# Performance work log

Measured on AMD Instinct MI355X. Metric: run time of the kernel, lower is better.

Reference implementation:

```python
import jax, jax.numpy as jnp
import numpy as np

B, N, E_PER = 512, 256, 8192          # graphs, nodes per graph, edges per graph
FIN, H, K, FOUT = 128, 32, 16, 10     # in_channels, hidden, num clusters, out_channels
EPS = 1e-15


def setup_inputs() -> dict:
    key = jax.random.key(0)
    ks = jax.random.split(key, 12)
    x = jax.random.normal(ks[0], (B * N, FIN), jnp.float32)
    # intra-graph random edges, then offset into the global node index space
    src = jax.random.randint(ks[1], (B, E_PER), 0, N)
    dst = jax.random.randint(ks[2], (B, E_PER), 0, N)
    offs = (jnp.arange(B) * N)[:, None]
    edge_index = jnp.stack([(src + offs).reshape(-1), (dst + offs).reshape(-1)]).astype(jnp.int64)
    batch = jnp.repeat(jnp.arange(B), N).astype(jnp.int64)

    def lin(k, fin, fout):
        return (jax.random.normal(k, (fin, fout), jnp.float32) / np.sqrt(fin)).astype(jnp.float32)

    params = {
        'W_lin1': lin(ks[3], FIN, H), 'b_lin1': jnp.zeros((H,), jnp.float32),
        'W_rel1': lin(ks[4], H, H), 'b_rel1': jnp.zeros((H,), jnp.float32),
        'W_root1': lin(ks[5], H, H),
        'W_pool': lin(ks[6], H, K), 'b_pool': jnp.zeros((K,), jnp.float32),
        'W_rel2': lin(ks[7], H, H), 'b_rel2': jnp.zeros((H,), jnp.float32),
        'W_root2': lin(ks[8], H, H),
        'W_lin2': lin(ks[9], H, H), 'b_lin2': jnp.zeros((H,), jnp.float32),
        'W_lin3': lin(ks[10], H, FOUT), 'b_lin3': jnp.zeros((FOUT,), jnp.float32),
    }
    return {'x': x, 'edge_index': edge_index, 'batch': batch, **params}


def _densify(x, edge_index, batch):
    """to_dense_adj + to_dense_batch: [total,F] -> [B,N,F], [B,N,N], [B,N]."""
    n_total = x.shape[0]
    counts = jax.ops.segment_sum(jnp.ones((n_total,), jnp.int32), batch, num_segments=B)
    offsets = jnp.concatenate([jnp.zeros((1,), jnp.int32), jnp.cumsum(counts)[:-1]])
    pos = jnp.arange(n_total) - offsets[batch]            # position of node inside its graph
    eb = batch[edge_index[0]]                             # graph id of each edge
    adj = jnp.zeros((B, N, N), jnp.float32).at[eb, pos[edge_index[0]], pos[edge_index[1]]].add(1.0)
    xd = jnp.zeros((B, N, x.shape[1]), jnp.float32).at[batch, pos].set(x)
    mask = jnp.zeros((B, N), jnp.float32).at[batch, pos].set(1.0)
    return xd, adj, mask


def _dense_graph_conv(x, adj, W_rel, b_rel, W_root):
    # PyG DenseGraphConv(aggr='add'): lin_rel(adj @ x) + lin_root(x)
    return jnp.einsum('bnm,bmh,hk->bnk', adj, x, W_rel) + b_rel + x @ W_root


def _dense_mincut_pool(x, adj, s, mask):
    s = jax.nn.softmax(s, axis=-1)
    x = x * mask[..., None]
    s = s * mask[..., None]
    out = jnp.einsum('bnk,bnh->bkh', s, x)                        # s^T x
    out_adj = jnp.einsum('bnk,bnm,bmj->bkj', s, adj, s)           # s^T A s
    mincut_num = jnp.einsum('bkk->b', out_adj)
    d_flat = adj.sum(-1)                                          # degree
    mincut_den = jnp.einsum('bnk,bn,bnk->b', s, d_flat, s)        # trace(s^T D s)
    mincut_loss = jnp.mean(-(mincut_num / mincut_den))
    ss = jnp.einsum('bnk,bnj->bkj', s, s)
    ss_norm = jnp.linalg.norm(ss, axis=(-1, -2), keepdims=True)
    i_s = jnp.eye(K, dtype=jnp.float32)
    ortho_loss = jnp.mean(jnp.linalg.norm(ss / ss_norm - i_s / jnp.sqrt(jnp.float32(K)), axis=(-1, -2)))
    # zero diagonal, symmetric degree normalization
    diag_mask = 1.0 - i_s
    out_adj = out_adj * diag_mask
    d = jnp.sqrt(out_adj.sum(-1))[:, None, :] + EPS               # [B,1,K]
    out_adj = out_adj / d / jnp.swapaxes(d, 1, 2)
    return out, out_adj, mincut_loss, ortho_loss


def reference(x, edge_index, batch, W_lin1, b_lin1, W_rel1, b_rel1, W_root1,
              W_pool, b_pool, W_rel2, b_rel2, W_root2, W_lin2, b_lin2, W_lin3, b_lin3):
    xd, adj, mask = _densify(x, edge_index, batch)
    h = xd @ W_lin1 + b_lin1                                      # lin1
    h = _dense_graph_conv(h, adj, W_rel1, b_rel1, W_root1)        # conv1
    s2 = h @ W_pool + b_pool                                      # pool2
    h, adj_p, mincut_loss2, ortho_loss2 = _dense_mincut_pool(h, adj, s2, mask)
    h = _dense_graph_conv(h, adj_p, W_rel2, b_rel2, W_root2)      # conv2
    h = h.sum(axis=1)                                             # readout sum over clusters
    h = jax.nn.relu(h @ W_lin2 + b_lin2)
    h = h @ W_lin3 + b_lin3
    return jax.nn.log_softmax(h, axis=-1), mincut_loss2, ortho_loss2
```

## Files before the change

kernel.cpp:

```cpp
#include <hip/hip_runtime.h>

#define NB 512
#define NN 256
#define EPG 8192
#define FINC 128

typedef float f32x4 __attribute__((ext_vector_type(4)));
typedef short s16x8 __attribute__((ext_vector_type(8)));

__device__ __forceinline__ float bf2f(unsigned short u) {
  union { unsigned int i; float f; } x; x.i = ((unsigned int)u) << 16; return x.f;
}
__device__ __forceinline__ unsigned short f2bf(float f) {
  union { float f; unsigned int i; } x; x.f = f;
  unsigned int r = x.i + 0x7fffu + ((x.i >> 16) & 1u);
  return (unsigned short)(r >> 16);
}
__device__ __forceinline__ short ftrunc_bf(float f) {
  union { float f; unsigned int i; } x; x.f = f;
  return (short)(x.i >> 16);
}

struct Params {
  const void* x; const void* ei;
  const void *wl1, *bl1, *wr1, *br1, *wro1, *wp, *bp;
  const void *wr2, *br2, *wro2, *wl2, *bl2, *wl3, *bl3;
  float* out; float* ws;
};

__device__ __forceinline__ bool detect_bf16(const void* p) {
  const unsigned short* pw = (const unsigned short*)p;
  int sane = 0;
  for (int i = 0; i < 64; ++i) {
    unsigned e = (pw[i] >> 7) & 0xFFu;
    sane += (e > 96u && e < 132u) ? 1 : 0;
  }
  return sane >= 56;
}
__device__ __forceinline__ bool detect_i64(const void* p) {
  const int* pi = (const int*)p + EPG;
  int ok = 0;
  for (int i = 0; i < 32; ++i) ok += (pi[i] >= 256 && pi[i] < 512) ? 1 : 0;
  return ok < 24;
}
__device__ __forceinline__ float ldf(const void* p, int i, bool bf) {
  return bf ? bf2f(((const unsigned short*)p)[i]) : ((const float*)p)[i];
}

#define SMEM_TOTAL 163072

__device__ __forceinline__ float block_sum16(float v, float* scr, int t) {
  #pragma unroll
  for (int o = 32; o > 0; o >>= 1) v += __shfl_xor(v, o, 64);
  __syncthreads();
  if ((t & 63) == 0) scr[t >> 6] = v;
  __syncthreads();
  float s = 0.f;
  #pragma unroll
  for (int i = 0; i < 16; ++i) s += scr[i];
  return s;
}

__global__ __launch_bounds__(1024, 4) void mincut_main(Params P) {
  extern __shared__ char smem[];
  const int t = threadIdx.x;
  const int b = blockIdx.x;

  const bool BF  = detect_bf16(P.wr1);
  const bool I64 = detect_i64(P.ei);

  float* h0buf  = (float*)(smem + 66560);
  unsigned short* taT = (unsigned short*)(smem + 66560);
  unsigned short* sTh = (unsigned short*)(smem + 66560 + 8448);
  unsigned short* sTl = (unsigned short*)(smem + 66560 + 16896);
  float* aggbuf = (float*)(smem + 103424);
  unsigned short* w1th = (unsigned short*)(smem + 103424);
  unsigned short* w1tl = (unsigned short*)(smem + 103424 + 8704);
  unsigned short* h0T  = (unsigned short*)(smem + 140288);
  unsigned short* wrelTh  = (unsigned short*)(smem + 140288);
  unsigned short* wrelTl  = (unsigned short*)(smem + 140288 + 2560);
  unsigned short* wrootTh = (unsigned short*)(smem + 140288 + 5120);
  float* brel1f = (float*)(smem + 140288 + 7680);
  unsigned short* h1Th = (unsigned short*)(smem + 140288);
  unsigned short* poolh = (unsigned short*)(smem + 160768);
  float* bpoolf = (float*)(smem + 160768 + 1024);
  float* blin1f = (float*)(smem + 160768 + 1088);
  float* scr    = (float*)(smem + 160768 + 1216);
  float* degb   = (float*)(smem + 160768 + 1280);
  float* pbuf   = (float*)(smem);
  float* oadjb  = (float*)(smem + 2048);
  float* ssb    = (float*)(smem + 3072);
  float* qbuf   = (float*)(smem + 4096);
  float* ddb    = (float*)(smem + 6144);
  float* h2b    = (float*)(smem + 6208);
  float* rb     = (float*)(smem + 8256);
  float* yb     = (float*)(smem + 8384);
  float* lgb    = (float*)(smem + 8512);
  float* rel2f  = (float*)(smem + 16384);
  float* brel2f = (float*)(smem + 20480);
  float* root2f = (float*)(smem + 20608);
  float* lin2f  = (float*)(smem + 24704);
  float* blin2f = (float*)(smem + 28800);
  float* lin3f  = (float*)(smem + 28928);
  float* blin3f = (float*)(smem + 30208);
  float* pbufH  = (float*)(smem + 40960);
  float* pbufL  = (float*)(smem + 43008);
  float* oadjH  = (float*)(smem + 45056);
  float* oadjL  = (float*)(smem + 46080);
  float* ssA    = (float*)(smem + 47104);
  float* ssB    = (float*)(smem + 48128);
  float* ssC    = (float*)(smem + 49152);

  const int n4 = t >> 2, q4 = t & 3;
  const int wv = t >> 6, lane = t & 63;
  const int lm = lane & 15, quad = lane >> 4;
  const int mbase = wv * 16;

  for (int e = t; e < 4096; e += 1024) {
    int k = e >> 5, c = e & 31;
    float w = ldf(P.wl1, e, BF);
    unsigned short hi = f2bf(w);
    w1th[c * 136 + k] = hi;
    w1tl[c * 136 + k] = f2bf(w - bf2f(hi));
  }
  if (t < 32) blin1f[t] = ldf(P.bl1, t, BF);
  if (t < 512) poolh[t] = f2bf(ldf(P.wp, t, BF));
  if (t < 16) bpoolf[t] = ldf(P.bp, t, BF);
  __syncthreads();

  {
    f32x4 acc[2] = {{0.f,0.f,0.f,0.f},{0.f,0.f,0.f,0.f}};
    const size_t node = (size_t)(b * 256 + mbase + lm);
    #pragma unroll
    for (int ks = 0; ks < 4; ++ks) {
      const int k0 = ks * 32 + quad * 8;
      s16x8 a;
      if (BF) {
        a = *(const s16x8*)((const unsigned short*)P.x + node * 128 + k0);
      } else {
        const float* xp = (const float*)P.x + node * 128 + k0;
        f32x4 v0 = *(const f32x4*)xp;
        f32x4 v1 = *(const f32x4*)(xp + 4);
        #pragma unroll
        for (int j = 0; j < 4; ++j) { a[j] = (short)f2bf(v0[j]); a[4 + j] = (short)f2bf(v1[j]); }
      }
      #pragma unroll
      for (int ct = 0; ct < 2; ++ct) {
        const int c = ct * 16 + lm;
        s16x8 bh = *(const s16x8*)(w1th + c * 136 + k0);
        s16x8 bl = *(const s16x8*)(w1tl + c * 136 + k0);
        acc[ct] = __builtin_amdgcn_mfma_f32_16x16x32_bf16(a, bh, acc[ct], 0, 0, 0);
        acc[ct] = __builtin_amdgcn_mfma_f32_16x16x32_bf16(a, bl, acc[ct], 0, 0, 0);
      }
    }
    #pragma unroll
    for (int ct = 0; ct < 2; ++ct) {
      const int c = ct * 16 + lm;
      float bias = blin1f[c];
      #pragma unroll
      for (int r = 0; r < 4; ++r) {
        int row = mbase + quad * 4 + r;
        float val = acc[ct][r] + bias;
        h0buf[row * 36 + c] = val;
        h0T[c * 264 + row] = f2bf(val);
      }
    }
  }
  __syncthreads();

  {
    uint4 z = {0u, 0u, 0u, 0u};
    for (int i = t; i < 4160; i += 1024) ((uint4*)smem)[i] = z;
  }
  __syncthreads();

  if (I64) {
    const long long* es = (const long long*)P.ei + (size_t)b * EPG;
    const long long* ed = (const long long*)P.ei + (size_t)NB * EPG + (size_t)b * EPG;
    #pragma unroll
    for (int i2 = 0; i2 < 8; ++i2) {
      int e = i2 * 1024 + t;
      unsigned idx = (unsigned)((((int)es[e]) & 255) * 260 + (((int)ed[e]) & 255));
      atomicAdd((unsigned int*)(smem + (idx & ~3u)), 1u << ((idx & 3u) * 8u));
    }
  } else {
    const int* es = (const int*)P.ei + (size_t)b * EPG;
    const int* ed = (const int*)P.ei + (size_t)NB * EPG + (size_t)b * EPG;
    #pragma unroll
    for (int i2 = 0; i2 < 8; ++i2) {
      int e = i2 * 1024 + t;
      unsigned idx = (unsigned)((es[e] & 255) * 260 + (ed[e] & 255));
      atomicAdd((unsigned int*)(smem + (idx & ~3u)), 1u << ((idx & 3u) * 8u));
    }
  }
  __syncthreads();

  s16x8 afr[8];
  {
    f32x4 acc[2] = {{0.f,0.f,0.f,0.f},{0.f,0.f,0.f,0.f}};
    float dsum = 0.f;
    #pragma unroll
    for (int ks = 0; ks < 8; ++ks) {
      const int v0 = ks * 32 + quad * 8;
      const char* ap = smem + (mbase + lm) * 260 + v0;
      unsigned d0 = *(const unsigned int*)(ap);
      unsigned d1 = *(const unsigned int*)(ap + 4);
      s16x8 a;
      #pragma unroll
      for (int j = 0; j < 4; ++j) {
        float f0 = (float)((d0 >> (8 * j)) & 255u);
        float f1 = (float)((d1 >> (8 * j)) & 255u);
        dsum += f0 + f1;
        a[j] = ftrunc_bf(f0);
        a[4 + j] = ftrunc_bf(f1);
      }
      afr[ks] = a;
      #pragma unroll
      for (int ct = 0; ct < 2; ++ct) {
        s16x8 bf = *(const s16x8*)(h0T + (ct * 16 + lm) * 264 + v0);
        acc[ct] = __builtin_amdgcn_mfma_f32_16x16x32_bf16(a, bf, acc[ct], 0, 0, 0);
      }
    }
    #pragma unroll
    for (int ct = 0; ct < 2; ++ct) {
      const int c = ct * 16 + lm;
      #pragma unroll
      for (int r = 0; r < 4; ++r) aggbuf[(mbase + quad * 4 + r) * 36 + c] = acc[ct][r];
    }
    dsum += __shfl_xor(dsum, 16, 64);
    dsum += __shfl_xor(dsum, 32, 64);
    if (lane < 16) degb[mbase + lm] = dsum;
  }
  __syncthreads();

  {
    int k = t >> 5, c = t & 31;
    float wr = ldf(P.wr1, t, BF);
    unsigned short hi = f2bf(wr);
    wrelTh[c * 40 + k] = hi;
    wrelTl[c * 40 + k] = f2bf(wr - bf2f(hi));
    wrootTh[c * 40 + k] = f2bf(ldf(P.wro1, t, BF));
  }
  if (t < 32) brel1f[t] = ldf(P.br1, t, BF);
  __syncthreads();

  f32x4 h1acc[2];
  float bias0, bias1;
  {
    s16x8 Ah, Al, Hh;
    const float* ar = aggbuf + (mbase + lm) * 36 + quad * 8;
    const float* hr = h0buf + (mbase + lm) * 36 + quad * 8;
    #pragma unroll
    for (int j = 0; j < 8; ++j) {
      float f = ar[j];
      unsigned short hi = f2bf(f);
      Ah[j] = (short)hi;
      Al[j] = (short)f2bf(f - bf2f(hi));
      Hh[j] = (short)f2bf(hr[j]);
    }
    bias0 = brel1f[lm]; bias1 = brel1f[16 + lm];
    #pragma unroll
    for (int ct = 0; ct < 2; ++ct) {
      const int c = ct * 16 + lm;
      s16x8 brh = *(const s16x8*)(wrelTh + c * 40 + quad * 8);
      s16x8 brl = *(const s16x8*)(wrelTl + c * 40 + quad * 8);
      s16x8 bwh = *(const s16x8*)(wrootTh + c * 40 + quad * 8);
      f32x4 acc = {0.f, 0.f, 0.f, 0.f};
      acc = __builtin_amdgcn_mfma_f32_16x16x32_bf16(Ah, brh, acc, 0, 0, 0);
      acc = __builtin_amdgcn_mfma_f32_16x16x32_bf16(Ah, brl, acc, 0, 0, 0);
      acc = __builtin_amdgcn_mfma_f32_16x16x32_bf16(Al, brh, acc, 0, 0, 0);
      acc = __builtin_amdgcn_mfma_f32_16x16x32_bf16(Hh, bwh, acc, 0, 0, 0);
      h1acc[ct] = acc;
    }
  }
  __syncthreads();
  {
    #pragma unroll
    for (int ct = 0; ct < 2; ++ct) {
      const int c = ct * 16 + lm;
      float bias = ct ? bias1 : bias0;
      #pragma unroll
      for (int r = 0; r < 4; ++r) {
        int row = mbase + quad * 4 + r;
        float val = h1acc[ct][r] + bias;
        aggbuf[row * 36 + c] = val;
        h1Th[c * 264 + row] = f2bf(val);
      }
    }
  }
  __syncthreads();

  float ssq;
  {
    f32x4 sv = *(const f32x4*)(bpoolf + q4 * 4);
    const float* hrow = aggbuf + n4 * 36;
    #pragma unroll 8
    for (int m = 0; m < 32; ++m) {
      float hm = hrow[m];
      uint2 pw = *(const uint2*)(poolh + m * 16 + q4 * 4);
      sv[0] += hm * bf2f((unsigned short)(pw.x & 0xFFFFu));
      sv[1] += hm * bf2f((unsigned short)(pw.x >> 16));
      sv[2] += hm * bf2f((unsigned short)(pw.y & 0xFFFFu));
      sv[3] += hm * bf2f((unsigned short)(pw.y >> 16));
    }
    float mx = fmaxf(fmaxf(sv[0], sv[1]), fmaxf(sv[2], sv[3]));
    mx = fmaxf(mx, __shfl_xor(mx, 1, 64));
    mx = fmaxf(mx, __shfl_xor(mx, 2, 64));
    #pragma unroll
    for (int i = 0; i < 4; ++i) sv[i] = __expf(sv[i] - mx);
    float sm = sv[0] + sv[1] + sv[2] + sv[3];
    sm += __shfl_xor(sm, 1, 64);
    sm += __shfl_xor(sm, 2, 64);
    float inv = 1.f / sm;
    #pragma unroll
    for (int i = 0; i < 4; ++i) sv[i] *= inv;
    float sq = sv[0] * sv[0] + sv[1] * sv[1] + sv[2] * sv[2] + sv[3] * sv[3];
    sq += __shfl_xor(sq, 1, 64);
    sq += __shfl_xor(sq, 2, 64);
    ssq = sq;
    #pragma unroll
    for (int i = 0; i < 4; ++i) {
      int cl = q4 * 4 + i;
      unsigned short hi = f2bf(sv[i]);
      sTh[cl * 264 + n4] = hi;
      sTl[cl * 264 + n4] = f2bf(sv[i] - bf2f(hi));
    }
  }
  __syncthreads();

  {
    f32x4 tacc = {0.f, 0.f, 0.f, 0.f};
    #pragma unroll
    for (int ks = 0; ks < 8; ++ks) {
      const int v0 = ks * 32 + quad * 8;
      s16x8 bh = *(const s16x8*)(sTh + lm * 264 + v0);
      s16x8 bl = *(const s16x8*)(sTl + lm * 264 + v0);
      tacc = __builtin_amdgcn_mfma_f32_16x16x32_bf16(afr[ks], bh, tacc, 0, 0, 0);
      tacc = __builtin_amdgcn_mfma_f32_16x16x32_bf16(afr[ks], bl, tacc, 0, 0, 0);
    }
    #pragma unroll
    for (int r = 0; r < 4; ++r) taT[lm * 264 + mbase + quad * 4 + r] = f2bf(tacc[r]);
  }
  __syncthreads();

  rel2f[t] = ldf(P.wr2, t, BF);
  if (t < 32) brel2f[t] = ldf(P.br2, t, BF);
  root2f[t] = ldf(P.wro2, t, BF);
  lin2f[t] = ldf(P.wl2, t, BF);
  if (t < 32) blin2f[t] = ldf(P.bl2, t, BF);
  if (t < 320) lin3f[t] = ldf(P.wl3, t, BF);
  if (t < 10) blin3f[t] = ldf(P.bl3, t, BF);

  if (wv < 9) {
    const unsigned short *Ap, *Bp; float* dst; int W, ct = 0;
    switch (wv) {
      case 0: Ap = sTh; Bp = h1Th; dst = pbufH; W = 32; ct = 0; break;
      case 1: Ap = sTh; Bp = h1Th; dst = pbufH; W = 32; ct = 1; break;
      case 2: Ap = sTl; Bp = h1Th; dst = pbufL; W = 32; ct = 0; break;
      case 3: Ap = sTl; Bp = h1Th; dst = pbufL; W = 32; ct = 1; break;
      case 4: Ap = sTh; Bp = taT;  dst = oadjH; W = 16; break;
      case 5: Ap = sTl; Bp = taT;  dst = oadjL; W = 16; break;
      case 6: Ap = sTh; Bp = sTh;  dst = ssA;   W = 16; break;
      case 7: Ap = sTh; Bp = sTl;  dst = ssB;   W = 16; break;
      default: Ap = sTl; Bp = sTh; dst = ssC;   W = 16; break;
    }
    const int cidx = ct * 16 + lm;
    const unsigned short* Bb = Bp + cidx * 264;
    f32x4 acc = {0.f, 0.f, 0.f, 0.f};
    #pragma unroll
    for (int ch = 0; ch < 8; ++ch) {
      s16x8 a = *(const s16x8*)(Ap + lm * 264 + ch * 32 + quad * 8);
      s16x8 bb = *(const s16x8*)(Bb + ch * 32 + quad * 8);
      acc = __builtin_amdgcn_mfma_f32_16x16x32_bf16(a, bb, acc, 0, 0, 0);
    }
    #pragma unroll
    for (int r = 0; r < 4; ++r) dst[(quad * 4 + r) * W + cidx] = acc[r];
  }
  __syncthreads();

  if (t < 512) {
    pbuf[t] = pbufH[t] + pbufL[t];
  } else if (t < 768) {
    int i = t - 512; oadjb[i] = oadjH[i] + oadjL[i];
  } else {
    int i = t - 768; ssb[i] = ssA[i] + ssB[i] + ssC[i];
  }
  __syncthreads();

  {
    float den = block_sum16((q4 == 0) ? degb[n4] * ssq : 0.f, scr, t);
    float num = block_sum16((t < 16) ? oadjb[t * 17] : 0.f, scr, t);
    float fro = block_sum16((t < 256) ? ssb[t] * ssb[t] : 0.f, scr, t);
    float ssn = sqrtf(fro);
    float term = 0.f;
    if (t < 256) {
      float diag = ((t & 15) == (t >> 4)) ? 0.25f : 0.f;
      term = ssb[t] / ssn - diag;
    }
    float orth = block_sum16(term * term, scr, t);
    if (t == 0) {
      atomicAdd(P.ws, -(num / den) * (1.f / NB));
      atomicAdd(P.ws + 1, sqrtf(orth) * (1.f / NB));
    }
  }
  __syncthreads();

  if (t < 16) {
    float rs = 0.f;
    #pragma unroll
    for (int j = 0; j < 16; ++j) if (j != t) rs += oadjb[t * 16 + j];
    ddb[t] = sqrtf(rs) + 1e-15f;
  }
  __syncthreads();
  if (t < 256) {
    int k = t >> 4, j = t & 15;
    float apv = (k == j) ? 0.f : oadjb[t] / (ddb[k] * ddb[j]);
    oadjb[t] = apv;
  }
  __syncthreads();

  if (t < 512) {
    int k = t >> 5, c = t & 31;
    float q = 0.f;
    #pragma unroll
    for (int j = 0; j < 16; ++j) q += oadjb[k * 16 + j] * pbuf[j * 32 + c];
    qbuf[k * 32 + c] = q;
  }
  __syncthreads();
  if (t < 512) {
    int k = t >> 5, c = t & 31;
    float a1 = brel2f[c];
    #pragma unroll
    for (int m = 0; m < 32; ++m)
      a1 += qbuf[k * 32 + m] * rel2f[m * 32 + c] + pbuf[k * 32 + m] * root2f[m * 32 + c];
    h2b[k * 32 + c] = a1;
  }
  __syncthreads();
  if (t < 32) {
    float r = 0.f;
    #pragma unroll
    for (int k = 0; k < 16; ++k) r += h2b[k * 32 + t];
    rb[t] = r;
  }
  __syncthreads();
  if (t < 32) {
    float y = blin2f[t];
    #pragma unroll
    for (int m = 0; m < 32; ++m) y += rb[m] * lin2f[m * 32 + t];
    yb[t] = fmaxf(y, 0.f);
  }
  __syncthreads();
  if (t < 10) {
    float lg = blin3f[t];
    #pragma unroll
    for (int m = 0; m < 32; ++m) lg += yb[m] * lin3f[m * 10 + t];
    lgb[t] = lg;
  }
  __syncthreads();
  if (t == 0) {
    float mx = lgb[0];
    #pragma unroll
    for (int i = 1; i < 10; ++i) mx = fmaxf(mx, lgb[i]);
    float sum = 0.f;
    #pragma unroll
    for (int i = 0; i < 10; ++i) sum += __expf(lgb[i] - mx);
    lgb[10] = mx + __logf(sum);
  }
  __syncthreads();
  if (t < 10) {
    float val = lgb[t] - lgb[10];
    if (BF) ((unsigned short*)P.out)[b * 10 + t] = f2bf(val);
    else    P.out[b * 10 + t] = val;
  }
}

__global__ void mincut_fin(Params P) {
  if (threadIdx.x == 0) {
    const bool BF = detect_bf16(P.wr1);
    if (BF) {
      ((unsigned short*)P.out)[5120] = f2bf(P.ws[0]);
      ((unsigned short*)P.out)[5121] = f2bf(P.ws[1]);
    } else {
      P.out[5120] = P.ws[0];
      P.out[5121] = P.ws[1];
    }
  }
}

extern "C" void kernel_launch(void* const* d_in, const int* in_sizes, int n_in,
                              void* d_out, int out_size, void* d_ws, size_t ws_size,
                              hipStream_t stream) {
  (void)in_sizes; (void)n_in; (void)out_size; (void)ws_size;
  Params P;
  P.x    = d_in[0];
  P.ei   = d_in[1];
  P.wl1  = d_in[3];
  P.bl1  = d_in[4];
  P.wr1  = d_in[5];
  P.br1  = d_in[6];
  P.wro1 = d_in[7];
  P.wp   = d_in[8];
  P.bp   = d_in[9];
  P.wr2  = d_in[10];
  P.br2  = d_in[11];
  P.wro2 = d_in[12];
  P.wl2  = d_in[13];
  P.bl2  = d_in[14];
  P.wl3  = d_in[15];
  P.bl3  = d_in[16];
  P.out  = (float*)d_out;
  P.ws   = (float*)d_ws;

  hipMemsetAsync(d_ws, 0, 2 * sizeof(float), stream);
  hipFuncSetAttribute(reinterpret_cast<const void*>(mincut_main),
                      hipFuncAttributeMaxDynamicSharedMemorySize, SMEM_TOTAL);
  hipLaunchKernelGGL(mincut_main, dim3(NB), dim3(1024), SMEM_TOTAL, stream, P);
  hipLaunchKernelGGL(mincut_fin, dim3(1), dim3(64), 0, stream, P);
}
```

Baseline: 196.5 us.

## Prefetch weights and edges early, MFMA pool softmax, fuse reductions and tail

Weights, biases and edge indices are loaded into registers at kernel start with vectorized edge reads. The adjacency zeroing and atomic scatter move ahead of the lin1 GEMM, which removes a couple of barriers. The pool projection becomes a split-bf16 MFMA with softmax done through wave shuffles. The four loss reductions are fused into a single cross-wave pass, and the ortho loss uses a closed-form trace identity. The classifier tail runs on one wave without block barriers. The adjacency row stride changes to 264, which alters the LDS layout.

```diff
diff --git a/kernel.cpp b/kernel.cpp
--- a/kernel.cpp
+++ b/kernel.cpp
@@ -47,19 +47,7 @@
   return bf ? bf2f(((const unsigned short*)p)[i]) : ((const float*)p)[i];
 }
 
-#define SMEM_TOTAL 163072
-
-__device__ __forceinline__ float block_sum16(float v, float* scr, int t) {
-  #pragma unroll
-  for (int o = 32; o > 0; o >>= 1) v += __shfl_xor(v, o, 64);
-  __syncthreads();
-  if ((t & 63) == 0) scr[t >> 6] = v;
-  __syncthreads();
-  float s = 0.f;
-  #pragma unroll
-  for (int i = 0; i < 16; ++i) s += scr[i];
-  return s;
-}
+#define SMEM_TOTAL 162752
 
 __global__ __launch_bounds__(1024, 4) void mincut_main(Params P) {
   extern __shared__ char smem[];
@@ -69,24 +57,26 @@
   const bool BF  = detect_bf16(P.wr1);
   const bool I64 = detect_i64(P.ei);
 
-  float* h0buf  = (float*)(smem + 66560);
-  unsigned short* taT = (unsigned short*)(smem + 66560);
-  unsigned short* sTh = (unsigned short*)(smem + 66560 + 8448);
-  unsigned short* sTl = (unsigned short*)(smem + 66560 + 16896);
-  float* aggbuf = (float*)(smem + 103424);
-  unsigned short* w1th = (unsigned short*)(smem + 103424);
-  unsigned short* w1tl = (unsigned short*)(smem + 103424 + 8704);
-  unsigned short* h0T  = (unsigned short*)(smem + 140288);
-  unsigned short* wrelTh  = (unsigned short*)(smem + 140288);
-  unsigned short* wrelTl  = (unsigned short*)(smem + 140288 + 2560);
-  unsigned short* wrootTh = (unsigned short*)(smem + 140288 + 5120);
-  float* brel1f = (float*)(smem + 140288 + 7680);
-  unsigned short* h1Th = (unsigned short*)(smem + 140288);
-  unsigned short* poolh = (unsigned short*)(smem + 160768);
-  float* bpoolf = (float*)(smem + 160768 + 1024);
-  float* blin1f = (float*)(smem + 160768 + 1088);
-  float* scr    = (float*)(smem + 160768 + 1216);
-  float* degb   = (float*)(smem + 160768 + 1280);
+  float* h0buf  = (float*)(smem + 67584);
+  unsigned short* taT = (unsigned short*)(smem + 67584);
+  unsigned short* sTh = (unsigned short*)(smem + 76032);
+  unsigned short* sTl = (unsigned short*)(smem + 84480);
+  float* aggbuf = (float*)(smem + 104448);
+  unsigned short* w1th = (unsigned short*)(smem + 104448);
+  unsigned short* w1tl = (unsigned short*)(smem + 113152);
+  unsigned short* h0T  = (unsigned short*)(smem + 141312);
+  unsigned short* wrelTh  = (unsigned short*)(smem + 141312);
+  unsigned short* wrelTl  = (unsigned short*)(smem + 143872);
+  unsigned short* wrootTh = (unsigned short*)(smem + 146432);
+  float* brel1f = (float*)(smem + 148992);
+  unsigned short* h1Th = (unsigned short*)(smem + 141312);
+  unsigned short* poolTh = (unsigned short*)(smem + 158208);
+  unsigned short* poolTl = (unsigned short*)(smem + 159232);
+  float* bpoolf = (float*)(smem + 160256);
+  float* blin1f = (float*)(smem + 160320);
+  float* scr    = (float*)(smem + 160448);
+  float* degb   = (float*)(smem + 160704);
+  float* ssqb   = (float*)(smem + 161728);
   float* pbuf   = (float*)(smem);
   float* oadjb  = (float*)(smem + 2048);
   float* ssb    = (float*)(smem + 3072);
@@ -97,12 +87,9 @@
   float* yb     = (float*)(smem + 8384);
   float* lgb    = (float*)(smem + 8512);
   float* rel2f  = (float*)(smem + 16384);
-  float* brel2f = (float*)(smem + 20480);
   float* root2f = (float*)(smem + 20608);
   float* lin2f  = (float*)(smem + 24704);
-  float* blin2f = (float*)(smem + 28800);
   float* lin3f  = (float*)(smem + 28928);
-  float* blin3f = (float*)(smem + 30208);
   float* pbufH  = (float*)(smem + 40960);
   float* pbufL  = (float*)(smem + 43008);
   float* oadjH  = (float*)(smem + 45056);
@@ -111,11 +98,45 @@
   float* ssB    = (float*)(smem + 48128);
   float* ssC    = (float*)(smem + 49152);
 
-  const int n4 = t >> 2, q4 = t & 3;
   const int wv = t >> 6, lane = t & 63;
   const int lm = lane & 15, quad = lane >> 4;
   const int mbase = wv * 16;
 
+  float wrel_v  = ldf(P.wr1, t, BF);
+  float wroot_v = ldf(P.wro1, t, BF);
+  float brel1_v = (t < 32) ? ldf(P.br1, t, BF) : 0.f;
+  float rel2_v  = ldf(P.wr2, t, BF);
+  float root2_v = ldf(P.wro2, t, BF);
+  float lin2_v  = ldf(P.wl2, t, BF);
+  float lin3_v  = (t < 320) ? ldf(P.wl3, t, BF) : 0.f;
+  float brel2_v = (t < 32) ? ldf(P.br2, t, BF) : 0.f;
+  float blin2_v = (t < 32) ? ldf(P.bl2, t, BF) : 0.f;
+  float blin3_v = (t < 10) ? ldf(P.bl3, t, BF) : 0.f;
+  int eu[8], ev[8];
+  if (I64) {
+    const uint4* s4 = (const uint4*)((const long long*)P.ei + (size_t)b * EPG) + t * 4;
+    const uint4* d4 = (const uint4*)((const long long*)P.ei + (size_t)NB * EPG + (size_t)b * EPG) + t * 4;
+    #pragma unroll
+    for (int i = 0; i < 4; ++i) {
+      uint4 a = s4[i], c = d4[i];
+      eu[2 * i] = a.x & 255; eu[2 * i + 1] = a.z & 255;
+      ev[2 * i] = c.x & 255; ev[2 * i + 1] = c.z & 255;
+    }
+  } else {
+    const uint4* s4 = (const uint4*)((const int*)P.ei + (size_t)b * EPG) + t * 2;
+    const uint4* d4 = (const uint4*)((const int*)P.ei + (size_t)NB * EPG + (size_t)b * EPG) + t * 2;
+    #pragma unroll
+    for (int i = 0; i < 2; ++i) {
+      uint4 a = s4[i], c = d4[i];
+      eu[4 * i] = a.x & 255; eu[4 * i + 1] = a.y & 255; eu[4 * i + 2] = a.z & 255; eu[4 * i + 3] = a.w & 255;
+      ev[4 * i] = c.x & 255; ev[4 * i + 1] = c.y & 255; ev[4 * i + 2] = c.z & 255; ev[4 * i + 3] = c.w & 255;
+    }
+  }
+
+  {
+    uint4 z = {0u, 0u, 0u, 0u};
+    for (int i = t; i < 4224; i += 1024) ((uint4*)smem)[i] = z;
+  }
   for (int e = t; e < 4096; e += 1024) {
     int k = e >> 5, c = e & 31;
     float w = ldf(P.wl1, e, BF);
@@ -123,10 +144,22 @@
     w1th[c * 136 + k] = hi;
     w1tl[c * 136 + k] = f2bf(w - bf2f(hi));
   }
+  if (t < 512) {
+    int m = t >> 4, c = t & 15;
+    float w = ldf(P.wp, t, BF);
+    unsigned short hi = f2bf(w);
+    poolTh[c * 32 + m] = hi;
+    poolTl[c * 32 + m] = f2bf(w - bf2f(hi));
+  }
   if (t < 32) blin1f[t] = ldf(P.bl1, t, BF);
-  if (t < 512) poolh[t] = f2bf(ldf(P.wp, t, BF));
   if (t < 16) bpoolf[t] = ldf(P.bp, t, BF);
   __syncthreads();
+
+  #pragma unroll
+  for (int e = 0; e < 8; ++e) {
+    unsigned idx = (unsigned)(eu[e] * 264 + ev[e]);
+    atomicAdd((unsigned int*)(smem + (idx & ~3u)), 1u << ((idx & 3u) * 8u));
+  }
 
   {
     f32x4 acc[2] = {{0.f,0.f,0.f,0.f},{0.f,0.f,0.f,0.f}};
@@ -168,48 +201,20 @@
   }
   __syncthreads();
 
-  {
-    uint4 z = {0u, 0u, 0u, 0u};
-    for (int i = t; i < 4160; i += 1024) ((uint4*)smem)[i] = z;
-  }
-  __syncthreads();
-
-  if (I64) {
-    const long long* es = (const long long*)P.ei + (size_t)b * EPG;
-    const long long* ed = (const long long*)P.ei + (size_t)NB * EPG + (size_t)b * EPG;
-    #pragma unroll
-    for (int i2 = 0; i2 < 8; ++i2) {
-      int e = i2 * 1024 + t;
-      unsigned idx = (unsigned)((((int)es[e]) & 255) * 260 + (((int)ed[e]) & 255));
-      atomicAdd((unsigned int*)(smem + (idx & ~3u)), 1u << ((idx & 3u) * 8u));
-    }
-  } else {
-    const int* es = (const int*)P.ei + (size_t)b * EPG;
-    const int* ed = (const int*)P.ei + (size_t)NB * EPG + (size_t)b * EPG;
-    #pragma unroll
-    for (int i2 = 0; i2 < 8; ++i2) {
-      int e = i2 * 1024 + t;
-      unsigned idx = (unsigned)((es[e] & 255) * 260 + (ed[e] & 255));
-      atomicAdd((unsigned int*)(smem + (idx & ~3u)), 1u << ((idx & 3u) * 8u));
-    }
-  }
-  __syncthreads();
-
   s16x8 afr[8];
   {
     f32x4 acc[2] = {{0.f,0.f,0.f,0.f},{0.f,0.f,0.f,0.f}};
     float dsum = 0.f;
+    const char* arow_ = smem + (mbase + lm) * 264;
     #pragma unroll
     for (int ks = 0; ks < 8; ++ks) {
       const int v0 = ks * 32 + quad * 8;
-      const char* ap = smem + (mbase + lm) * 260 + v0;
-      unsigned d0 = *(const unsigned int*)(ap);
-      unsigned d1 = *(const unsigned int*)(ap + 4);
+      uint2 d = *(const uint2*)(arow_ + v0);
       s16x8 a;
       #pragma unroll
       for (int j = 0; j < 4; ++j) {
-        float f0 = (float)((d0 >> (8 * j)) & 255u);
-        float f1 = (float)((d1 >> (8 * j)) & 255u);
+        float f0 = (float)((d.x >> (8 * j)) & 255u);
+        float f1 = (float)((d.y >> (8 * j)) & 255u);
         dsum += f0 + f1;
         a[j] = ftrunc_bf(f0);
         a[4 + j] = ftrunc_bf(f1);
@@ -235,13 +240,12 @@
 
   {
     int k = t >> 5, c = t & 31;
-    float wr = ldf(P.wr1, t, BF);
-    unsigned short hi = f2bf(wr);
+    unsigned short hi = f2bf(wrel_v);
     wrelTh[c * 40 + k] = hi;
-    wrelTl[c * 40 + k] = f2bf(wr - bf2f(hi));
-    wrootTh[c * 40 + k] = f2bf(ldf(P.wro1, t, BF));
-  }
-  if (t < 32) brel1f[t] = ldf(P.br1, t, BF);
+    wrelTl[c * 40 + k] = f2bf(wrel_v - bf2f(hi));
+    wrootTh[c * 40 + k] = f2bf(wroot_v);
+  }
+  if (t < 32) brel1f[t] = brel1_v;
   __syncthreads();
 
   f32x4 h1acc[2];
@@ -288,42 +292,60 @@
       }
     }
   }
-  __syncthreads();
-
-  float ssq;
-  {
-    f32x4 sv = *(const f32x4*)(bpoolf + q4 * 4);
-    const float* hrow = aggbuf + n4 * 36;
-    #pragma unroll 8
-    for (int m = 0; m < 32; ++m) {
-      float hm = hrow[m];
-      uint2 pw = *(const uint2*)(poolh + m * 16 + q4 * 4);
-      sv[0] += hm * bf2f((unsigned short)(pw.x & 0xFFFFu));
-      sv[1] += hm * bf2f((unsigned short)(pw.x >> 16));
-      sv[2] += hm * bf2f((unsigned short)(pw.y & 0xFFFFu));
-      sv[3] += hm * bf2f((unsigned short)(pw.y >> 16));
-    }
-    float mx = fmaxf(fmaxf(sv[0], sv[1]), fmaxf(sv[2], sv[3]));
-    mx = fmaxf(mx, __shfl_xor(mx, 1, 64));
-    mx = fmaxf(mx, __shfl_xor(mx, 2, 64));
-    #pragma unroll
-    for (int i = 0; i < 4; ++i) sv[i] = __expf(sv[i] - mx);
-    float sm = sv[0] + sv[1] + sv[2] + sv[3];
-    sm += __shfl_xor(sm, 1, 64);
-    sm += __shfl_xor(sm, 2, 64);
-    float inv = 1.f / sm;
-    #pragma unroll
-    for (int i = 0; i < 4; ++i) sv[i] *= inv;
-    float sq = sv[0] * sv[0] + sv[1] * sv[1] + sv[2] * sv[2] + sv[3] * sv[3];
-    sq += __shfl_xor(sq, 1, 64);
-    sq += __shfl_xor(sq, 2, 64);
-    ssq = sq;
-    #pragma unroll
-    for (int i = 0; i < 4; ++i) {
-      int cl = q4 * 4 + i;
-      unsigned short hi = f2bf(sv[i]);
-      sTh[cl * 264 + n4] = hi;
-      sTl[cl * 264 + n4] = f2bf(sv[i] - bf2f(hi));
+  {
+    s16x8 Ah, Al;
+    const float* hr = aggbuf + (mbase + lm) * 36 + quad * 8;
+    #pragma unroll
+    for (int j = 0; j < 8; ++j) {
+      float f = hr[j];
+      unsigned short hi = f2bf(f);
+      Ah[j] = (short)hi;
+      Al[j] = (short)f2bf(f - bf2f(hi));
+    }
+    s16x8 Bh = *(const s16x8*)(poolTh + lm * 32 + quad * 8);
+    s16x8 Bl = *(const s16x8*)(poolTl + lm * 32 + quad * 8);
+    f32x4 lg = {0.f, 0.f, 0.f, 0.f};
+    lg = __builtin_amdgcn_mfma_f32_16x16x32_bf16(Ah, Bh, lg, 0, 0, 0);
+    lg = __builtin_amdgcn_mfma_f32_16x16x32_bf16(Al, Bh, lg, 0, 0, 0);
+    lg = __builtin_amdgcn_mfma_f32_16x16x32_bf16(Ah, Bl, lg, 0, 0, 0);
+    float bp = bpoolf[lm];
+    #pragma unroll
+    for (int r = 0; r < 4; ++r) lg[r] += bp;
+    f32x4 mx = lg;
+    #pragma unroll
+    for (int m = 1; m <= 8; m <<= 1) {
+      #pragma unroll
+      for (int r = 0; r < 4; ++r) mx[r] = fmaxf(mx[r], __shfl_xor(mx[r], m, 64));
+    }
+    #pragma unroll
+    for (int r = 0; r < 4; ++r) lg[r] = __expf(lg[r] - mx[r]);
+    f32x4 sm = lg;
+    #pragma unroll
+    for (int m = 1; m <= 8; m <<= 1) {
+      #pragma unroll
+      for (int r = 0; r < 4; ++r) sm[r] += __shfl_xor(sm[r], m, 64);
+    }
+    f32x4 sq;
+    #pragma unroll
+    for (int r = 0; r < 4; ++r) {
+      lg[r] = lg[r] / sm[r];
+      sq[r] = lg[r] * lg[r];
+    }
+    #pragma unroll
+    for (int m = 1; m <= 8; m <<= 1) {
+      #pragma unroll
+      for (int r = 0; r < 4; ++r) sq[r] += __shfl_xor(sq[r], m, 64);
+    }
+    #pragma unroll
+    for (int r = 0; r < 4; ++r) {
+      int node = mbase + quad * 4 + r;
+      unsigned short hi = f2bf(lg[r]);
+      sTh[lm * 264 + node] = hi;
+      sTl[lm * 264 + node] = f2bf(lg[r] - bf2f(hi));
+    }
+    if (lm == 0) {
+      #pragma unroll
+      for (int r = 0; r < 4; ++r) ssqb[mbase + quad * 4 + r] = sq[r];
     }
   }
   __syncthreads();
@@ -343,13 +365,10 @@
   }
   __syncthreads();
 
-  rel2f[t] = ldf(P.wr2, t, BF);
-  if (t < 32) brel2f[t] = ldf(P.br2, t, BF);
-  root2f[t] = ldf(P.wro2, t, BF);
-  lin2f[t] = ldf(P.wl2, t, BF);
-  if (t < 32) blin2f[t] = ldf(P.bl2, t, BF);
-  if (t < 320) lin3f[t] = ldf(P.wl3, t, BF);
-  if (t < 10) blin3f[t] = ldf(P.bl3, t, BF);
+  rel2f[t] = rel2_v;
+  root2f[t] = root2_v;
+  lin2f[t] = lin2_v;
+  if (t < 320) lin3f[t] = lin3_v;
 
   if (wv < 9) {
     const unsigned short *Ap, *Bp; float* dst; int W, ct = 0;
@@ -388,23 +407,29 @@
   __syncthreads();
 
   {
-    float den = block_sum16((q4 == 0) ? degb[n4] * ssq : 0.f, scr, t);
-    float num = block_sum16((t < 16) ? oadjb[t * 17] : 0.f, scr, t);
-    float fro = block_sum16((t < 256) ? ssb[t] * ssb[t] : 0.f, scr, t);
+    float vden = (t < 256) ? degb[t] * ssqb[t] : 0.f;
+    float vnum = (t < 16) ? oadjb[t * 17] : 0.f;
+    float vfro = (t < 256) ? ssb[t] * ssb[t] : 0.f;
+    float vtr  = (t < 16) ? ssb[t * 17] : 0.f;
+    #pragma unroll
+    for (int o = 32; o > 0; o >>= 1) {
+      vden += __shfl_xor(vden, o, 64);
+      vnum += __shfl_xor(vnum, o, 64);
+      vfro += __shfl_xor(vfro, o, 64);
+      vtr  += __shfl_xor(vtr, o, 64);
+    }
+    if (lane == 0) { scr[wv] = vden; scr[16 + wv] = vnum; scr[32 + wv] = vfro; scr[48 + wv] = vtr; }
+  }
+  __syncthreads();
+  if (t == 0) {
+    float den = 0.f, num = 0.f, fro = 0.f, tr = 0.f;
+    #pragma unroll
+    for (int i = 0; i < 16; ++i) { den += scr[i]; num += scr[16 + i]; fro += scr[32 + i]; tr += scr[48 + i]; }
     float ssn = sqrtf(fro);
-    float term = 0.f;
-    if (t < 256) {
-      float diag = ((t & 15) == (t >> 4)) ? 0.25f : 0.f;
-      term = ssb[t] / ssn - diag;
-    }
-    float orth = block_sum16(term * term, scr, t);
-    if (t == 0) {
-      atomicAdd(P.ws, -(num / den) * (1.f / NB));
-      atomicAdd(P.ws + 1, sqrtf(orth) * (1.f / NB));
-    }
-  }
-  __syncthreads();
-
+    float orth2 = 2.f - tr / (2.f * ssn);
+    atomicAdd(P.ws, -(num / den) * (1.f / NB));
+    atomicAdd(P.ws + 1, sqrtf(fmaxf(orth2, 0.f)) * (1.f / NB));
+  }
   if (t < 16) {
     float rs = 0.f;
     #pragma unroll
@@ -429,48 +454,53 @@
   __syncthreads();
   if (t < 512) {
     int k = t >> 5, c = t & 31;
-    float a1 = brel2f[c];
+    float a1 = brel2_v;
+    a1 = ((float*)nullptr == nullptr) ? a1 : a1;
+    float acc = (t < 32) ? 0.f : 0.f;
+    (void)acc;
+    float s0 = 0.f;
     #pragma unroll
     for (int m = 0; m < 32; ++m)
-      a1 += qbuf[k * 32 + m] * rel2f[m * 32 + c] + pbuf[k * 32 + m] * root2f[m * 32 + c];
-    h2b[k * 32 + c] = a1;
-  }
-  __syncthreads();
-  if (t < 32) {
-    float r = 0.f;
-    #pragma unroll
-    for (int k = 0; k < 16; ++k) r += h2b[k * 32 + t];
-    rb[t] = r;
-  }
-  __syncthreads();
-  if (t < 32) {
-    float y = blin2f[t];
-    #pragma unroll
-    for (int m = 0; m < 32; ++m) y += rb[m] * lin2f[m * 32 + t];
-    yb[t] = fmaxf(y, 0.f);
-  }
-  __syncthreads();
-  if (t < 10) {
-    float lg = blin3f[t];
-    #pragma unroll
-    for (int m = 0; m < 32; ++m) lg += yb[m] * lin3f[m * 10 + t];
-    lgb[t] = lg;
-  }
-  __syncthreads();
-  if (t == 0) {
-    float mx = lgb[0];
-    #pragma unroll
-    for (int i = 1; i < 10; ++i) mx = fmaxf(mx, lgb[i]);
-    float sum = 0.f;
-    #pragma unroll
-    for (int i = 0; i < 10; ++i) sum += __expf(lgb[i] - mx);
-    lgb[10] = mx + __logf(sum);
-  }
-  __syncthreads();
-  if (t < 10) {
-    float val = lgb[t] - lgb[10];
-    if (BF) ((unsigned short*)P.out)[b * 10 + t] = f2bf(val);
-    else    P.out[b * 10 + t] = val;
+      s0 += qbuf[k * 32 + m] * rel2f[m * 32 + c] + pbuf[k * 32 + m] * root2f[m * 32 + c];
+    h2b[k * 32 + c] = s0;
+  }
+  __syncthreads();
+
+  if (wv == 0) {
+    if (lane < 32) {
+      float r = 32.f * brel2_v;
+      r = 0.f;
+      #pragma unroll
+      for (int k = 0; k < 16; ++k) r += h2b[k * 32 + lane];
+      r += 16.f * brel2_v;
+      rb[lane] = r;
+    }
+    if (lane < 32) {
+      float y = blin2_v;
+      #pragma unroll
+      for (int m = 0; m < 32; ++m) y += rb[m] * lin2f[m * 32 + lane];
+      yb[lane] = fmaxf(y, 0.f);
+    }
+    if (lane < 10) {
+      float lg = blin3_v;
+      #pragma unroll
+      for (int m = 0; m < 32; ++m) lg += yb[m] * lin3f[m * 10 + lane];
+      lgb[lane] = lg;
+    }
+    if (lane == 0) {
+      float mx = lgb[0];
+      #pragma unroll
+      for (int i = 1; i < 10; ++i) mx = fmaxf(mx, lgb[i]);
+      float sum = 0.f;
+      #pragma unroll
+      for (int i = 0; i < 10; ++i) sum += __expf(lgb[i] - mx);
+      lgb[10] = mx + __logf(sum);
+    }
+    if (lane < 10) {
+      float val = lgb[lane] - lgb[10];
+      if (BF) ((unsigned short*)P.out)[b * 10 + lane] = f2bf(val);
+      else    P.out[b * 10 + lane] = val;
+    }
   }
 }
 
```

Result: faster. 182.6 us (-7.1%).
